# Performance work log

Measured on AMD Instinct MI355X. Metric: run time of the kernel, lower is better.

The kernel has to match this reference:

```python
import jax, jax.numpy as jnp
import numpy as np

B, L, C, H, W = 4, 8, 32, 128, 256
M1, M2 = 32, 32  # spectral modes


def setup_inputs() -> dict:
    key = jax.random.key(0)
    k1, k2, k3, k4, k5, k6 = jax.random.split(key, 6)
    scale = 1.0 / (C * C)
    return {
        "x": jax.random.normal(k1, (B, L, C, H, W), dtype=jnp.float32),
        "k": jax.random.normal(k2, (C, H, W), dtype=jnp.float32),
        "w1r": scale * jax.random.normal(k3, (C, C, M1, M2), dtype=jnp.float32),
        "w1i": scale * jax.random.normal(k4, (C, C, M1, M2), dtype=jnp.float32),
        "w2r": scale * jax.random.normal(k5, (C, C, M1, M2), dtype=jnp.float32),
        "w2i": scale * jax.random.normal(k6, (C, C, M1, M2), dtype=jnp.float32),
    }


def reference(x, k, w1r, w1i, w2r, w2i):
    # x: [B, L, C, H, W] real; k: [C, H, W] conv kernel (broadcast over B*L).
    b, l, c, h, w = x.shape
    # --- FlashFFTConvInterface fallback path: circular conv via rfft2.
    # H, W are already 2/3/5-smooth (next_fast_len is identity -> no padding).
    u = x.reshape(b * l, c, h, w)
    u_f = jnp.fft.rfft2(u)                     # [B*L, C, H, W//2+1] complex
    k_f = jnp.fft.rfft2(k)                     # [C, H, W//2+1], broadcasts
    y = jnp.fft.irfft2(u_f * k_f, s=(h, w)).reshape(b, l, c, h, w)

    # --- SpectralConv2d: per-mode channel mixing in frequency domain.
    x_f = jnp.fft.rfft2(y)                     # [B, L, C, H, Wf] complex
    wf = x_f.shape[-1]
    w1 = (w1r + 1j * w1i).astype(x_f.dtype)
    w2 = (w2r + 1j * w2i).astype(x_f.dtype)
    m1 = min(h, M1)
    m2 = min(wf, M2)
    co = w1.shape[1]
    top = jnp.einsum('blcij,coij->bloij', x_f[:, :, :, :m1, :m2], w1[:, :, :m1, :m2])
    out_f = jnp.zeros((b, l, co, h, wf), dtype=x_f.dtype)
    out_f = out_f.at[:, :, :, :m1, :m2].set(top)
    if h > 1 and (h > M1 or wf > M2):
        bot = jnp.einsum('blcij,coij->bloij', x_f[:, :, :, h - m1:, :m2], w2[:, :, :m1, :m2])
        out_f = out_f.at[:, :, :, h - m1:, :m2].set(bot)
    return jnp.fft.irfft2(out_f, s=(h, w))    # [B, L, Co, H, W] real
```

## Files before the change

### kernel.cpp

```cpp
#include <hip/hip_runtime.h>
#include <math.h>

#define Hn 128
#define Wn 256
#define PLANE (Hn*Wn)

#define OFF_TQC 0u
#define OFF_TQS 2048u
#define OFF_TP  4096u
#define OFF_KM  16384u
#define OFF_XM  147456u
#define OFF_B   4341760u
#define OFF_RK  12730368u

__global__ __launch_bounds__(256) void build_tables(float* __restrict__ ws) {
  int tid = blockIdx.x * 256 + threadIdx.x;
  const double PI2 = 6.283185307179586476925286766559;
  if (tid < 512) {
    int j = tid >> 4, xi = tid & 15;
    float cc[4], ss[4];
#pragma unroll
    for (int m = 0; m < 4; m++) {
      int x = xi * 4 + m;
      double ang = PI2 * (double)((j * x) & 255) / 256.0;
      cc[m] = (float)cos(ang); ss[m] = (float)sin(ang);
    }
    ((float4*)(ws + OFF_TQC))[tid] = make_float4(cc[0], cc[1], cc[2], cc[3]);
    ((float4*)(ws + OFF_TQS))[tid] = make_float4(ss[0], ss[1], ss[2], ss[3]);
  }
  if (tid < 2048) {
    int p = tid >> 6, y2 = tid & 63;
    double a0 = PI2 * (double)((p * (2 * y2)) & 127) / 128.0;
    double a1 = PI2 * (double)((p * (2 * y2 + 1)) & 127) / 128.0;
    ((float4*)(ws + OFF_TP))[tid] =
        make_float4((float)cos(a0), (float)sin(a0), (float)cos(a1), (float)sin(a1));
  }
}

__global__ __launch_bounds__(256, 3) void fwd_rows(const float* __restrict__ src,
                                                   float2* __restrict__ R,
                                                   const float* __restrict__ ws) {
  int plane = blockIdx.x >> 2, chunk = blockIdx.x & 3;
  __shared__ __align__(16) float Sd[32 * 260];
  __shared__ float4 Tc[544], Ts[544];
  int t = threadIdx.x;
  const float4* src4 = (const float4*)src;
  size_t sb = (size_t)plane * 8192 + (size_t)chunk * 2048;
#pragma unroll
  for (int k = 0; k < 8; k++) {
    int idx = t + 256 * k;
    int row = idx >> 6, c4 = idx & 63;
    int sws = (row >> 1) & 15;
    *(float4*)&Sd[row * 260 + ((c4 ^ sws) << 2)] = src4[sb + idx];
  }
  const float4* gTc = (const float4*)(ws + OFF_TQC);
  const float4* gTs = (const float4*)(ws + OFF_TQS);
#pragma unroll
  for (int k = 0; k < 2; k++) {
    int idx = t + 256 * k;
    Tc[(idx >> 4) * 17 + (idx & 15)] = gTc[idx];
    Ts[(idx >> 4) * 17 + (idx & 15)] = gTs[idx];
  }
  __syncthreads();
  float eA[4][4], oA[4][4];
#pragma unroll
  for (int uu = 0; uu < 4; uu++) {
    int unit = uu * 256 + t;
    int y = unit >> 5, xb = unit & 31;
    int sws = (y >> 1) & 15;
    const float* rowp = &Sd[y * 260];
    float4 A = *(const float4*)&rowp[(xb ^ sws) << 2];
    float Av[4] = {A.x, A.y, A.z, A.w};
    float M[4];
#pragma unroll
    for (int kk = 0; kk < 4; kk++) {
      int xm = 256 - 4 * xb - kk;
      int xmc = (xm > 255) ? 255 : xm;
      int c4m = xmc >> 2, e = xmc & 3;
      float v = rowp[((c4m ^ sws) << 2) + e];
      M[kk] = (xm > 255) ? 0.f : v;
    }
#pragma unroll
    for (int kk = 0; kk < 4; kk++) {
      eA[uu][kk] = Av[kk] + M[kk];
      oA[uu][kk] = Av[kk] - M[kk];
    }
    if (xb == 0) {
      oA[uu][0] = rowp[(32 ^ sws) << 2];
    }
  }
  __syncthreads();
#pragma unroll
  for (int uu = 0; uu < 4; uu++) {
    int unit = uu * 256 + t;
    int y = unit >> 5, xb = unit & 31;
    int sws = (y >> 1) & 15;
    float* rowp = &Sd[y * 260];
    *(float4*)&rowp[(xb ^ sws) << 2] =
        make_float4(eA[uu][0], eA[uu][1], eA[uu][2], eA[uu][3]);
    *(float4*)&rowp[((32 + xb) ^ sws) << 2] =
        make_float4(oA[uu][0], oA[uu][1], oA[uu][2], oA[uu][3]);
  }
  __syncthreads();
  int jg = t & 15, yg = t >> 4;
  int jm = jg & 3;
  const float4* pC0 = &Tc[jg * 17];
  const float4* pS0 = &Ts[jg * 17];
  const float4* pC1 = &Tc[(jg + 16) * 17];
  const float4* pS1 = &Ts[(jg + 16) * 17];
  const float4* p2_0 = (jm & 1) ? pS0 : pC0;
  const float4* p4_0 = (jm & 1) ? pC0 : pS0;
  const float4* p2_1 = (jm & 1) ? pS1 : pC1;
  const float4* p4_1 = (jm & 1) ? pC1 : pS1;
  float sa = (jm == 0 || jm == 3) ? 1.f : -1.f;
  float sb_ = (jm < 2) ? 1.f : -1.f;
  float pm = (jg & 1) ? -1.f : 1.f;
  int sw = yg & 15;
  const float* row0 = &Sd[(2 * yg) * 260];
  const float* row1 = &Sd[(2 * yg + 1) * 260];
  float d1[2][2], d2[2][2], d3[2][2], d4[2][2];
#pragma unroll
  for (int a = 0; a < 2; a++)
#pragma unroll
    for (int b = 0; b < 2; b++) { d1[a][b] = 0.f; d2[a][b] = 0.f; d3[a][b] = 0.f; d4[a][b] = 0.f; }
#define DOT4(a, b) (a.x * b.x + a.y * b.y + a.z * b.z + a.w * b.w)
#pragma unroll 4
  for (int xb = 0; xb < 16; xb++) {
    int off = (xb ^ sw) << 2;
    float4 e0y0 = *(const float4*)&row0[off];
    float4 e1y0 = *(const float4*)&row0[off + 64];
    float4 o0y0 = *(const float4*)&row0[off + 128];
    float4 o1y0 = *(const float4*)&row0[off + 192];
    float4 e0y1 = *(const float4*)&row1[off];
    float4 e1y1 = *(const float4*)&row1[off + 64];
    float4 o0y1 = *(const float4*)&row1[off + 128];
    float4 o1y1 = *(const float4*)&row1[off + 192];
    float4 c0 = pC0[xb], s0 = pS0[xb];
    float4 t20 = p2_0[xb], t40 = p4_0[xb];
    float4 c1 = pC1[xb], s1 = pS1[xb];
    float4 t21 = p2_1[xb], t41 = p4_1[xb];
    d1[0][0] += DOT4(e0y0, c0);  d1[0][1] += DOT4(e0y1, c0);
    d1[1][0] += DOT4(e0y0, c1);  d1[1][1] += DOT4(e0y1, c1);
    d2[0][0] += DOT4(e1y0, t20); d2[0][1] += DOT4(e1y1, t20);
    d2[1][0] += DOT4(e1y0, t21); d2[1][1] += DOT4(e1y1, t21);
    d3[0][0] += DOT4(o0y0, s0);  d3[0][1] += DOT4(o0y1, s0);
    d3[1][0] += DOT4(o0y0, s1);  d3[1][1] += DOT4(o0y1, s1);
    d4[0][0] += DOT4(o1y0, t40); d4[0][1] += DOT4(o1y1, t40);
    d4[1][0] += DOT4(o1y0, t41); d4[1][1] += DOT4(o1y1, t41);
  }
#undef DOT4
  float u128_0 = row0[128 + 4 * sw];
  float u128_1 = row1[128 + 4 * sw];
#pragma unroll
  for (int jj = 0; jj < 2; jj++) {
    int j = jg + 16 * jj;
#pragma unroll
    for (int ky = 0; ky < 2; ky++) {
      int y = chunk * 32 + yg * 2 + ky;
      float u128 = ky ? u128_1 : u128_0;
      float re = d1[jj][ky] + sa * d2[jj][ky] + pm * u128;
      float im = -(d3[jj][ky] + sb_ * d4[jj][ky]);
      R[((size_t)plane * 128 + y) * 32 + j] = make_float2(re, im);
    }
  }
}

__global__ __launch_bounds__(256) void fwd_cols(const float2* __restrict__ Rg,
                                                float2* __restrict__ dst,
                                                const float* __restrict__ ws) {
  int plane = blockIdx.x;
  __shared__ float4 Rs4[2048];
  __shared__ float4 TPs[2048];
  float2* Rs = (float2*)Rs4;
  int t = threadIdx.x;
  const float4* in4 = (const float4*)(Rg + (size_t)plane * 4096);
#pragma unroll
  for (int k = 0; k < 8; k++) Rs4[t + 256 * k] = in4[t + 256 * k];
  const float4* gTP = (const float4*)(ws + OFF_TP);
#pragma unroll
  for (int k = 0; k < 8; k++) TPs[t + 256 * k] = gTP[t + 256 * k];
  __syncthreads();
  int j = t & 31, pg = t >> 5;
  float Are[4], Aim[4], Bre[4], Bim[4];
#pragma unroll
  for (int m = 0; m < 4; m++) { Are[m] = Aim[m] = Bre[m] = Bim[m] = 0.f; }
  for (int it = 0; it < 32; it++) {
#pragma unroll
    for (int h = 0; h < 2; h++) {
      int y2 = 2 * it + h;
      float sg = (h == 0) ? 1.f : -1.f;
      float2 r0 = Rs[(2 * y2) * 32 + j];
      float2 r1 = Rs[(2 * y2 + 1) * 32 + j];
#pragma unroll
      for (int m = 0; m < 4; m++) {
        int p = pg + 8 * m;
        float4 tw = TPs[p * 64 + y2];
        float P0 = r0.x * tw.x + r0.y * tw.y;
        float Q0 = r0.y * tw.x - r0.x * tw.y;
        float P1 = r1.x * tw.z + r1.y * tw.w;
        float Q1 = r1.y * tw.z - r1.x * tw.w;
        Are[m] += P0 + P1;
        Aim[m] += Q0 + Q1;
        Bre[m] += sg * (P0 - Q1);
        Bim[m] += sg * (Q0 + P1);
      }
    }
  }
  size_t ob = (size_t)plane * 2048;
#pragma unroll
  for (int m = 0; m < 4; m++) {
    int p = pg + 8 * m;
    dst[ob + p * 32 + j] = make_float2(Are[m], Aim[m]);
    dst[ob + (32 + p) * 32 + j] = make_float2(Bre[m], Bim[m]);
  }
}

__global__ __launch_bounds__(256) void wk_build(const float* __restrict__ w1r,
                                                const float* __restrict__ w1i,
                                                const float* __restrict__ w2r,
                                                const float* __restrict__ w2i,
                                                float2* __restrict__ wk,
                                                const float2* __restrict__ km) {
  int e0 = blockIdx.x * 256 + threadIdx.x;
#pragma unroll
  for (int k = 0; k < 4; k++) {
    int e = e0 + k * 524288;
    int o = e & 31, c = (e >> 5) & 31, j = (e >> 10) & 31, i64 = e >> 15;
    int r = (i64 < 32) ? i64 : i64 - 32;
    const float* wr = (i64 < 32) ? w1r : w2r;
    const float* wi = (i64 < 32) ? w1i : w2i;
    int widx = ((c * 32 + o) * 32 + r) * 32 + j;
    float wrv = wr[widx], wiv = wi[widx];
    float2 kv = km[(size_t)c * 2048 + i64 * 32 + j];
    wk[e] = make_float2(kv.x * wrv - kv.y * wiv, kv.x * wiv + kv.y * wrv);
  }
}

__global__ __launch_bounds__(256) void mix_modes(float2* __restrict__ xm,
                                                 const float2* __restrict__ wk) {
  int bid = blockIdx.x;
  int mode = (bid & 7) * 256 + (bid >> 3);
  __shared__ float4 Xs4[512], Ws4[512];
  float2* Xs = (float2*)Xs4;
  float2* Wsl = (float2*)Ws4;
  int t = threadIdx.x;
#pragma unroll
  for (int k = 0; k < 4; k++) {
    int p = t + 256 * k;
    Xs[p] = xm[(size_t)p * 2048 + mode];
  }
  const float4* wk4 = (const float4*)(wk + (size_t)mode * 1024);
#pragma unroll
  for (int k = 0; k < 2; k++) Ws4[t + 256 * k] = wk4[t + 256 * k];
  __syncthreads();
  int o = t & 31, bg = t >> 5;
  float orr[4], oii[4];
#pragma unroll
  for (int m = 0; m < 4; m++) { orr[m] = 0.f; oii[m] = 0.f; }
  for (int c2 = 0; c2 < 16; c2++) {
    float2 w0 = Wsl[(2 * c2) * 32 + o];
    float2 w1 = Wsl[(2 * c2 + 1) * 32 + o];
#pragma unroll
    for (int m = 0; m < 4; m++) {
      float4 xv = *(const float4*)&Xs[(bg * 4 + m) * 32 + 2 * c2];
      orr[m] += xv.x * w0.x - xv.y * w0.y + xv.z * w1.x - xv.w * w1.y;
      oii[m] += xv.x * w0.y + xv.y * w0.x + xv.z * w1.y + xv.w * w1.x;
    }
  }
#pragma unroll
  for (int m = 0; m < 4; m++)
    xm[(size_t)((bg * 4 + m) * 32 + o) * 2048 + mode] = make_float2(orr[m], oii[m]);
}

__global__ __launch_bounds__(256) void inv_rows(const float2* __restrict__ om,
                                                float2* __restrict__ G,
                                                const float* __restrict__ ws) {
  int plane = blockIdx.x;
  __shared__ float4 Os4[1024];
  __shared__ float4 TPs[2048];
  float2* Os = (float2*)Os4;
  int t = threadIdx.x;
  const float4* in4 = (const float4*)(om + (size_t)plane * 2048);
#pragma unroll
  for (int k = 0; k < 4; k++) Os4[t + 256 * k] = in4[t + 256 * k];
  const float4* gTP = (const float4*)(ws + OFF_TP);
#pragma unroll
  for (int k = 0; k < 8; k++) TPs[t + 256 * k] = gTP[t + 256 * k];
  __syncthreads();
  int j = t & 31, yg = t >> 5;
  float gr[16], gi[16];
#pragma unroll
  for (int k = 0; k < 16; k++) { gr[k] = 0.f; gi[k] = 0.f; }
  for (int p = 0; p < 32; p++) {
    float2 A = Os[p * 32 + j];
    float2 B = Os[(32 + p) * 32 + j];
#pragma unroll
    for (int mp = 0; mp < 8; mp++) {
      int y2 = yg * 8 + mp;
      float4 tw = TPs[p * 64 + y2];
      float sg = ((mp & 1) == 0) ? 1.f : -1.f;
      float Sr = A.x + sg * B.x, Si = A.y + sg * B.y;
      gr[2 * mp]     += Sr * tw.x - Si * tw.y;
      gi[2 * mp]     += Sr * tw.y + Si * tw.x;
      float Tr = A.x + sg * B.y, Ti = A.y - sg * B.x;
      gr[2 * mp + 1] += Tr * tw.z - Ti * tw.w;
      gi[2 * mp + 1] += Tr * tw.w + Ti * tw.z;
    }
  }
  const float inv = 1.0f / 32768.0f;
  size_t gb = (size_t)plane * 128;
#pragma unroll
  for (int mm = 0; mm < 16; mm++) {
    int y = yg * 16 + mm;
    float sr = (j == 0) ? gr[mm] * inv : 2.f * inv * gr[mm];
    float si = (j == 0) ? 0.f : 2.f * inv * gi[mm];
    G[(gb + y) * 32 + j] = make_float2(sr, si);
  }
}

__global__ __launch_bounds__(256) void inv_cols(const float2* __restrict__ G,
                                                float* __restrict__ out,
                                                const float* __restrict__ ws) {
  int plane = blockIdx.x >> 2, chunk = blockIdx.x & 3;
  __shared__ float2 Gs[32 * 33];
  __shared__ float4 Tc[544], Ts[544];
  int t = threadIdx.x;
  const float2* in = G + (size_t)plane * 4096 + (size_t)chunk * 1024;
#pragma unroll
  for (int k = 0; k < 4; k++) {
    int idx = t + 256 * k;
    Gs[(idx >> 5) * 33 + (idx & 31)] = in[idx];
  }
  const float4* gTc = (const float4*)(ws + OFF_TQC);
  const float4* gTs = (const float4*)(ws + OFF_TQS);
#pragma unroll
  for (int k = 0; k < 2; k++) {
    int idx = t + 256 * k;
    Tc[(idx >> 4) * 17 + (idx & 15)] = gTc[idx];
    Ts[(idx >> 4) * 17 + (idx & 15)] = gTs[idx];
  }
  __syncthreads();
  int xi = t & 15, yg = t >> 4;
  float4 Ce[2], Co[2], Se[2], So[2];
  float c64[2], s64[2];
#pragma unroll
  for (int ky = 0; ky < 2; ky++) {
    Ce[ky] = make_float4(0.f, 0.f, 0.f, 0.f);
    Co[ky] = make_float4(0.f, 0.f, 0.f, 0.f);
    Se[ky] = make_float4(0.f, 0.f, 0.f, 0.f);
    So[ky] = make_float4(0.f, 0.f, 0.f, 0.f);
    c64[ky] = 0.f; s64[ky] = 0.f;
  }
#define FMA4(acc, s, v) do { acc.x += (s) * (v).x; acc.y += (s) * (v).y; \
                             acc.z += (s) * (v).z; acc.w += (s) * (v).w; } while (0)
#pragma unroll 4
  for (int jh = 0; jh < 16; jh++) {
    float4 ce = Tc[(2 * jh) * 17 + xi],     se = Ts[(2 * jh) * 17 + xi];
    float4 co = Tc[(2 * jh + 1) * 17 + xi], so = Ts[(2 * jh + 1) * 17 + xi];
    float sgn = (jh & 1) ? -1.f : 1.f;
#pragma unroll
    for (int ky = 0; ky < 2; ky++) {
      float2 ge = Gs[(yg * 2 + ky) * 33 + 2 * jh];
      float2 go = Gs[(yg * 2 + ky) * 33 + 2 * jh + 1];
      FMA4(Ce[ky], ge.x, ce);
      FMA4(Se[ky], ge.y, se);
      FMA4(Co[ky], go.x, co);
      FMA4(So[ky], go.y, so);
      c64[ky] += sgn * ge.x;
      s64[ky] += sgn * go.y;
    }
  }
#undef FMA4
  float* outp = out + (size_t)plane * PLANE + (size_t)chunk * 32 * Wn;
#pragma unroll
  for (int ky = 0; ky < 2; ky++) {
    int y = yg * 2 + ky;
    float* ro = outp + y * Wn;
    float4 C  = make_float4(Ce[ky].x + Co[ky].x, Ce[ky].y + Co[ky].y,
                            Ce[ky].z + Co[ky].z, Ce[ky].w + Co[ky].w);
    float4 Cm = make_float4(Ce[ky].x - Co[ky].x, Ce[ky].y - Co[ky].y,
                            Ce[ky].z - Co[ky].z, Ce[ky].w - Co[ky].w);
    float4 S  = make_float4(Se[ky].x + So[ky].x, Se[ky].y + So[ky].y,
                            Se[ky].z + So[ky].z, Se[ky].w + So[ky].w);
    float4 Sm = make_float4(So[ky].x - Se[ky].x, So[ky].y - Se[ky].y,
                            So[ky].z - Se[ky].z, So[ky].w - Se[ky].w);
    *(float4*)(ro + 4 * xi) =
        make_float4(C.x - S.x, C.y - S.y, C.z - S.z, C.w - S.w);
    *(float4*)(ro + 128 + 4 * xi) =
        make_float4(Cm.x + Sm.x, Cm.y + Sm.y, Cm.z + Sm.z, Cm.w + Sm.w);
    int mb = 128 - 4 * xi;
    ro[mb]     = Cm.x - Sm.x;
    ro[mb - 1] = Cm.y - Sm.y;
    ro[mb - 2] = Cm.z - Sm.z;
    ro[mb - 3] = Cm.w - Sm.w;
    int nb = 256 - 4 * xi;
    if (xi) ro[nb] = C.x + S.x;
    ro[nb - 1] = C.y + S.y;
    ro[nb - 2] = C.z + S.z;
    ro[nb - 3] = C.w + S.w;
    if (xi == 0) {
      ro[64]  = c64[ky] - s64[ky];
      ro[192] = c64[ky] + s64[ky];
    }
  }
}

extern "C" void kernel_launch(void* const* d_in, const int* in_sizes, int n_in,
                              void* d_out, int out_size, void* d_ws, size_t ws_size,
                              hipStream_t stream) {
  (void)in_sizes; (void)n_in; (void)out_size; (void)ws_size;
  const float* x   = (const float*)d_in[0];
  const float* kk  = (const float*)d_in[1];
  const float* w1r = (const float*)d_in[2];
  const float* w1i = (const float*)d_in[3];
  const float* w2r = (const float*)d_in[4];
  const float* w2i = (const float*)d_in[5];
  float*  ws   = (float*)d_ws;
  float*  out  = (float*)d_out;
  float2* km2  = (float2*)(ws + OFF_KM);
  float2* xm2  = (float2*)(ws + OFF_XM);
  float2* bx   = (float2*)(ws + OFF_B);
  float2* rk   = (float2*)(ws + OFF_RK);

  build_tables<<<8, 256, 0, stream>>>(ws);
  fwd_rows<<<4096, 256, 0, stream>>>(x, bx, ws);
  fwd_rows<<<128, 256, 0, stream>>>(kk, rk, ws);
  fwd_cols<<<1024, 256, 0, stream>>>(bx, xm2, ws);
  fwd_cols<<<32, 256, 0, stream>>>(rk, km2, ws);
  wk_build<<<2048, 256, 0, stream>>>(w1r, w1i, w2r, w2i, bx, km2);
  mix_modes<<<2048, 256, 0, stream>>>(xm2, bx);
  inv_rows<<<1024, 256, 0, stream>>>(xm2, bx, ws);
  inv_cols<<<4096, 256, 0, stream>>>(bx, out, ws);
}
```

Baseline: 425.3 us.

## Add second even/odd folding level to forward row DFT to halve dot products

The forward row DFT in fwd_rows now folds each row twice using x to 128-x symmetry as well as x to 256-x, splitting inputs into four quarter-length vectors chosen by the parity of the output frequency. Each thread then needs only one cosine and one sine dot product per frequency instead of four. Special terms at indices 64 and 128 are stored separately, and the shared row stride grows to fit them. This cuts the FLOPs and LDS reads of the inner loop, at the cost of more complex preprocessing and a larger shared buffer.

```diff
diff --git a/kernel.cpp b/kernel.cpp
--- a/kernel.cpp
+++ b/kernel.cpp
@@ -37,11 +37,12 @@
   }
 }
 
+#define RS 276
 __global__ __launch_bounds__(256, 3) void fwd_rows(const float* __restrict__ src,
                                                    float2* __restrict__ R,
                                                    const float* __restrict__ ws) {
   int plane = blockIdx.x >> 2, chunk = blockIdx.x & 3;
-  __shared__ __align__(16) float Sd[32 * 260];
+  __shared__ __align__(16) float Sd[32 * RS];
   __shared__ float4 Tc[544], Ts[544];
   int t = threadIdx.x;
   const float4* src4 = (const float4*)src;
@@ -51,7 +52,7 @@
     int idx = t + 256 * k;
     int row = idx >> 6, c4 = idx & 63;
     int sws = (row >> 1) & 15;
-    *(float4*)&Sd[row * 260 + ((c4 ^ sws) << 2)] = src4[sb + idx];
+    *(float4*)&Sd[row * RS + ((c4 ^ sws) << 2)] = src4[sb + idx];
   }
   const float4* gTc = (const float4*)(ws + OFF_TQC);
   const float4* gTs = (const float4*)(ws + OFF_TQS);
@@ -62,108 +63,117 @@
     Ts[(idx >> 4) * 17 + (idx & 15)] = gTs[idx];
   }
   __syncthreads();
-  float eA[4][4], oA[4][4];
-#pragma unroll
-  for (int uu = 0; uu < 4; uu++) {
+  float EPv[2][4], EMv[2][4], OPv[2][4], OMv[2][4];
+  float spE64[2], spU128[2], spO64[2];
+#pragma unroll
+  for (int uu = 0; uu < 2; uu++) {
     int unit = uu * 256 + t;
-    int y = unit >> 5, xb = unit & 31;
+    int y = unit >> 4, xq = unit & 15;
     int sws = (y >> 1) & 15;
-    const float* rowp = &Sd[y * 260];
-    float4 A = *(const float4*)&rowp[(xb ^ sws) << 2];
-    float Av[4] = {A.x, A.y, A.z, A.w};
-    float M[4];
+    const float* rowp = &Sd[y * RS];
+    float4 A0 = *(const float4*)&rowp[(xq ^ sws) << 2];
+    float4 A2 = *(const float4*)&rowp[((32 + xq) ^ sws) << 2];
+    float Av0[4] = {A0.x, A0.y, A0.z, A0.w};
+    float Av2[4] = {A2.x, A2.y, A2.z, A2.w};
+    float M1[4], M2[4];
 #pragma unroll
     for (int kk = 0; kk < 4; kk++) {
-      int xm = 256 - 4 * xb - kk;
-      int xmc = (xm > 255) ? 255 : xm;
-      int c4m = xmc >> 2, e = xmc & 3;
-      float v = rowp[((c4m ^ sws) << 2) + e];
-      M[kk] = (xm > 255) ? 0.f : v;
+      int s1 = 128 - 4 * xq - kk;
+      M1[kk] = rowp[(((s1 >> 2) ^ sws) << 2) + (s1 & 3)];
+      int s2 = 256 - 4 * xq - kk;
+      int s2c = (s2 > 255) ? 255 : s2;
+      M2[kk] = rowp[(((s2c >> 2) ^ sws) << 2) + (s2c & 3)];
     }
 #pragma unroll
     for (int kk = 0; kk < 4; kk++) {
-      eA[uu][kk] = Av[kk] + M[kk];
-      oA[uu][kk] = Av[kk] - M[kk];
-    }
-    if (xb == 0) {
-      oA[uu][0] = rowp[(32 ^ sws) << 2];
-    }
-  }
-  __syncthreads();
-#pragma unroll
-  for (int uu = 0; uu < 4; uu++) {
+      float a = Av0[kk] + M2[kk], b = Av0[kk] - M2[kk];
+      float c = M1[kk] + Av2[kk], d = M1[kk] - Av2[kk];
+      EPv[uu][kk] = a + c;  EMv[uu][kk] = a - c;
+      OPv[uu][kk] = b + d;  OMv[uu][kk] = b - d;
+    }
+    spE64[uu] = 0.f; spU128[uu] = 0.f; spO64[uu] = 0.f;
+    if (xq == 0) {
+      EPv[uu][0] = Av0[0];  EMv[uu][0] = Av0[0];
+      OPv[uu][0] = 0.f;     OMv[uu][0] = 0.f;
+      float u64v  = rowp[((16 ^ sws) << 2)];
+      float u192v = rowp[((48 ^ sws) << 2)];
+      spE64[uu]  = u64v + u192v;
+      spO64[uu]  = u64v - u192v;
+      spU128[uu] = Av2[0];
+    }
+  }
+  __syncthreads();
+#pragma unroll
+  for (int uu = 0; uu < 2; uu++) {
     int unit = uu * 256 + t;
-    int y = unit >> 5, xb = unit & 31;
+    int y = unit >> 4, xq = unit & 15;
     int sws = (y >> 1) & 15;
-    float* rowp = &Sd[y * 260];
-    *(float4*)&rowp[(xb ^ sws) << 2] =
-        make_float4(eA[uu][0], eA[uu][1], eA[uu][2], eA[uu][3]);
-    *(float4*)&rowp[((32 + xb) ^ sws) << 2] =
-        make_float4(oA[uu][0], oA[uu][1], oA[uu][2], oA[uu][3]);
+    float* rowp = &Sd[y * RS];
+    int off = (xq ^ sws) << 2;
+    *(float4*)&rowp[off]       = make_float4(EPv[uu][0], EPv[uu][1], EPv[uu][2], EPv[uu][3]);
+    *(float4*)&rowp[68 + off]  = make_float4(EMv[uu][0], EMv[uu][1], EMv[uu][2], EMv[uu][3]);
+    *(float4*)&rowp[136 + off] = make_float4(OMv[uu][0], OMv[uu][1], OMv[uu][2], OMv[uu][3]);
+    *(float4*)&rowp[204 + off] = make_float4(OPv[uu][0], OPv[uu][1], OPv[uu][2], OPv[uu][3]);
+    if (xq == 0) {
+      rowp[64] = spE64[uu];
+      rowp[65] = spU128[uu];
+      rowp[66] = spO64[uu];
+    }
   }
   __syncthreads();
   int jg = t & 15, yg = t >> 4;
-  int jm = jg & 3;
+  int jodd = jg & 1;
+  int aC = jodd ? 68 : 0;
+  int aS = jodd ? 204 : 136;
   const float4* pC0 = &Tc[jg * 17];
   const float4* pS0 = &Ts[jg * 17];
   const float4* pC1 = &Tc[(jg + 16) * 17];
   const float4* pS1 = &Ts[(jg + 16) * 17];
-  const float4* p2_0 = (jm & 1) ? pS0 : pC0;
-  const float4* p4_0 = (jm & 1) ? pC0 : pS0;
-  const float4* p2_1 = (jm & 1) ? pS1 : pC1;
-  const float4* p4_1 = (jm & 1) ? pC1 : pS1;
-  float sa = (jm == 0 || jm == 3) ? 1.f : -1.f;
-  float sb_ = (jm < 2) ? 1.f : -1.f;
-  float pm = (jg & 1) ? -1.f : 1.f;
-  int sw = yg & 15;
-  const float* row0 = &Sd[(2 * yg) * 260];
-  const float* row1 = &Sd[(2 * yg + 1) * 260];
-  float d1[2][2], d2[2][2], d3[2][2], d4[2][2];
+  float sgE = jodd ? 0.f : (((jg >> 1) & 1) ? -1.f : 1.f);
+  float sgO = jodd ? ((((jg - 1) >> 1) & 1) ? -1.f : 1.f) : 0.f;
+  float pm = jodd ? -1.f : 1.f;
+  int sw = yg;
+  const float* row0 = &Sd[(2 * yg) * RS];
+  const float* row1 = &Sd[(2 * yg + 1) * RS];
+  float dc[2][2], dsn[2][2];
 #pragma unroll
   for (int a = 0; a < 2; a++)
 #pragma unroll
-    for (int b = 0; b < 2; b++) { d1[a][b] = 0.f; d2[a][b] = 0.f; d3[a][b] = 0.f; d4[a][b] = 0.f; }
+    for (int b = 0; b < 2; b++) { dc[a][b] = 0.f; dsn[a][b] = 0.f; }
 #define DOT4(a, b) (a.x * b.x + a.y * b.y + a.z * b.z + a.w * b.w)
 #pragma unroll 4
   for (int xb = 0; xb < 16; xb++) {
     int off = (xb ^ sw) << 2;
-    float4 e0y0 = *(const float4*)&row0[off];
-    float4 e1y0 = *(const float4*)&row0[off + 64];
-    float4 o0y0 = *(const float4*)&row0[off + 128];
-    float4 o1y0 = *(const float4*)&row0[off + 192];
-    float4 e0y1 = *(const float4*)&row1[off];
-    float4 e1y1 = *(const float4*)&row1[off + 64];
-    float4 o0y1 = *(const float4*)&row1[off + 128];
-    float4 o1y1 = *(const float4*)&row1[off + 192];
+    float4 eY0 = *(const float4*)&row0[aC + off];
+    float4 eY1 = *(const float4*)&row1[aC + off];
+    float4 oY0 = *(const float4*)&row0[aS + off];
+    float4 oY1 = *(const float4*)&row1[aS + off];
     float4 c0 = pC0[xb], s0 = pS0[xb];
-    float4 t20 = p2_0[xb], t40 = p4_0[xb];
     float4 c1 = pC1[xb], s1 = pS1[xb];
-    float4 t21 = p2_1[xb], t41 = p4_1[xb];
-    d1[0][0] += DOT4(e0y0, c0);  d1[0][1] += DOT4(e0y1, c0);
-    d1[1][0] += DOT4(e0y0, c1);  d1[1][1] += DOT4(e0y1, c1);
-    d2[0][0] += DOT4(e1y0, t20); d2[0][1] += DOT4(e1y1, t20);
-    d2[1][0] += DOT4(e1y0, t21); d2[1][1] += DOT4(e1y1, t21);
-    d3[0][0] += DOT4(o0y0, s0);  d3[0][1] += DOT4(o0y1, s0);
-    d3[1][0] += DOT4(o0y0, s1);  d3[1][1] += DOT4(o0y1, s1);
-    d4[0][0] += DOT4(o1y0, t40); d4[0][1] += DOT4(o1y1, t40);
-    d4[1][0] += DOT4(o1y0, t41); d4[1][1] += DOT4(o1y1, t41);
+    dc[0][0] += DOT4(eY0, c0);  dc[0][1] += DOT4(eY1, c0);
+    dc[1][0] += DOT4(eY0, c1);  dc[1][1] += DOT4(eY1, c1);
+    dsn[0][0] += DOT4(oY0, s0); dsn[0][1] += DOT4(oY1, s0);
+    dsn[1][0] += DOT4(oY0, s1); dsn[1][1] += DOT4(oY1, s1);
   }
 #undef DOT4
-  float u128_0 = row0[128 + 4 * sw];
-  float u128_1 = row1[128 + 4 * sw];
+  float E64_0 = row0[64], u128_0 = row0[65], O64_0 = row0[66];
+  float E64_1 = row1[64], u128_1 = row1[65], O64_1 = row1[66];
 #pragma unroll
   for (int jj = 0; jj < 2; jj++) {
     int j = jg + 16 * jj;
 #pragma unroll
     for (int ky = 0; ky < 2; ky++) {
       int y = chunk * 32 + yg * 2 + ky;
+      float E64 = ky ? E64_1 : E64_0;
       float u128 = ky ? u128_1 : u128_0;
-      float re = d1[jj][ky] + sa * d2[jj][ky] + pm * u128;
-      float im = -(d3[jj][ky] + sb_ * d4[jj][ky]);
+      float O64 = ky ? O64_1 : O64_0;
+      float re = dc[jj][ky] + sgE * E64 + pm * u128;
+      float im = -dsn[jj][ky] - sgO * O64;
       R[((size_t)plane * 128 + y) * 32 + j] = make_float2(re, im);
     }
   }
 }
+#undef RS
 
 __global__ __launch_bounds__(256) void fwd_cols(const float2* __restrict__ Rg,
                                                 float2* __restrict__ dst,
```

Measured after the change: 417.9 us. About the same (-1.7%).
